# Kernel optimization log

Measured on AMD Instinct MI355X. Metric: run time of the kernel, lower is better.

The kernel has to match this reference:

```python
import jax, jax.numpy as jnp
import numpy as np

B, T, E, H = 2, 2048, 1024, 16  # batch, seq(block_size), n_embed, n_head


def setup_inputs() -> dict:
    key = jax.random.key(0)
    kx, kq, kk, kv, kf = jax.random.split(key, 5)
    s = 0.02
    return {
        "x": jax.random.normal(kx, (B, T, E), jnp.float32),
        "Wq": jax.random.normal(kq, (E, E), jnp.float32) * s,
        "Wk": jax.random.normal(kk, (E, E), jnp.float32) * s,
        "Wv": jax.random.normal(kv, (E, E), jnp.float32) * s,
        "Wf": jax.random.normal(kf, (E, E), jnp.float32) * s,
        "bf": jnp.zeros((E,), jnp.float32),
    }


def reference(x, Wq, Wk, Wv, Wf, bf):
    b, t, e = x.shape
    dh = e // H
    # per-head projections (no bias), heads concatenated along feature dim
    q = (x @ Wq).reshape(b, t, H, dh)
    k = (x @ Wk).reshape(b, t, H, dh)
    v = (x @ Wv).reshape(b, t, H, dh)
    # NOTE: original scales by sqrt(full embed dim C), not sqrt(head_size)
    scores = jnp.einsum("bqhd,bkhd->bhqk", q, k) / jnp.sqrt(jnp.asarray(e, x.dtype))
    causal = jnp.tril(jnp.ones((t, t), bool))
    scores = jnp.where(causal, scores, -jnp.inf)
    wei = jax.nn.softmax(scores, axis=-1)
    attn = jnp.einsum("bhqk,bkhd->bqhd", wei, v).reshape(b, t, e)
    x = x + attn  # residual (no out-projection in original)
    # FeedForward: single Linear + ReLU, residual
    return x + jnp.maximum(x @ Wf + bf, 0)
```

## Files before the change

kernel.cpp:

```cpp
#include <hip/hip_runtime.h>
#include <cstdint>
#include <cstddef>

typedef unsigned short u16;
typedef short short8 __attribute__((ext_vector_type(8)));
typedef float floatx4 __attribute__((ext_vector_type(4)));

__device__ __forceinline__ float bf2f(u16 u) {
    union { unsigned int i; float f; } v; v.i = ((unsigned int)u) << 16; return v.f;
}
__device__ __forceinline__ u16 f2bf(float f) {
    union { float f; unsigned int i; } v; v.f = f;
    unsigned int u = v.i;
    return (u16)((u + 0x7fffu + ((u >> 16) & 1u)) >> 16);
}

#if __has_builtin(__builtin_amdgcn_exp2f)
#define EXP2F(x) __builtin_amdgcn_exp2f(x)
#else
#define EXP2F(x) exp2f(x)
#endif

__device__ __forceinline__ void gload_lds16(const u16* g, void* lds_wave_base) {
    __builtin_amdgcn_global_load_lds(
        (__attribute__((address_space(1))) void*)g,
        (__attribute__((address_space(3))) void*)lds_wave_base,
        16, 0, 0);
}

#define WAITVM(N) asm volatile("s_waitcnt vmcnt(" #N ")" ::: "memory")
#define BARRIER_ACQ()                      \
    do {                                   \
        __builtin_amdgcn_s_barrier();      \
        asm volatile("" ::: "memory");     \
        __builtin_amdgcn_sched_barrier(0); \
    } while (0)
#define BARRIER_REL()                      \
    do {                                   \
        asm volatile("" ::: "memory");     \
        __builtin_amdgcn_s_barrier();      \
    } while (0)

__global__ void conv_transpose_k(const float* __restrict__ w0, const float* __restrict__ w1,
                                 const float* __restrict__ w2, const float* __restrict__ w3,
                                 u16* __restrict__ o0, u16* __restrict__ o1,
                                 u16* __restrict__ o2, u16* __restrict__ o3, int n) {
    __shared__ float t[32][33];
    const float* w; u16* o;
    switch (blockIdx.z) {
        case 0: w = w0; o = o0; break;
        case 1: w = w1; o = o1; break;
        case 2: w = w2; o = o2; break;
        default: w = w3; o = o3; break;
    }
    int tx = threadIdx.x, ty = threadIdx.y;
    int x0 = blockIdx.x * 32, y0 = blockIdx.y * 32;
    t[ty][tx] = w[(size_t)(y0 + ty) * n + x0 + tx];
    __syncthreads();
    o[(size_t)(x0 + ty) * n + y0 + tx] = f2bf(t[tx][ty]);
}

__global__ void conv_k(const float* __restrict__ in, u16* __restrict__ out, int n) {
    int i = (blockIdx.x * blockDim.x + threadIdx.x) * 4;
    if (i >= n) return;
    float4 v = *(const float4*)&in[i];
    ushort4 o;
    o.x = f2bf(v.x); o.y = f2bf(v.y); o.z = f2bf(v.z); o.w = f2bf(v.w);
    *(ushort4*)&out[i] = o;
}

#define QSTG(K0, BUF)                                                          \
    {                                                                          \
        _Pragma("unroll")                                                      \
        for (int it = 0; it < 2; ++it) {                                       \
            int idx = it * 256 + tid;                                          \
            int row = idx >> 2;                                                \
            int c8 = (idx & 3) * 8;                                            \
            size_t ldsoff = (size_t)(it * 256 + wave * 64) * 16;               \
            gload_lds16(&A[(size_t)(bm + row) * K + (K0) + c8],                \
                        (char*)smem + (BUF) * 8192 + ldsoff);                  \
            gload_lds16(&Bt[(size_t)(bn + row) * K + (K0) + c8],               \
                        (char*)smem + 16384 + (BUF) * 8192 + ldsoff);          \
        }                                                                      \
    }

__global__ __launch_bounds__(256, 3) void gemm_qkv(
    const u16* __restrict__ A, const u16* __restrict__ Bt,
    u16* __restrict__ qpk, u16* __restrict__ kpk, u16* __restrict__ vpk,
    int M, int T, int K) {
    __shared__ __align__(16) u16 smem[16384];

    const int tid = threadIdx.x;
    const int lane = tid & 63, wave = tid >> 6;
    const int wm = (wave >> 1) * 64, wn = (wave & 1) * 64;
    const int bm = blockIdx.x * 128, bn = blockIdx.y * 128;
    const int l15 = lane & 15, lq = lane >> 4;

    const int sec = bn >> 10;
    u16* dst = (sec == 0) ? qpk : (sec == 1) ? kpk : vpk;
    const int bnE = bn & 1023;

    floatx4 acc[4][4];
#pragma unroll
    for (int i = 0; i < 4; ++i)
#pragma unroll
        for (int j = 0; j < 4; ++j) acc[i][j] = (floatx4)0.0f;

    const int nkt = K / 32;
    QSTG(0, 0);

    for (int kt = 0; kt < nkt; ++kt) {
        const int cur = kt & 1;
        if (kt + 1 < nkt) {
            QSTG((kt + 1) * 32, cur ^ 1);
            WAITVM(4);
        } else {
            WAITVM(0);
        }
        BARRIER_ACQ();

        const u16* la = smem + cur * 4096;
        const u16* lb = smem + 8192 + cur * 4096;
        short8 af[4], bfr[4];
#pragma unroll
        for (int i = 0; i < 4; ++i) af[i] = *(const short8*)&la[(wm + i * 16 + l15) * 32 + lq * 8];
#pragma unroll
        for (int j = 0; j < 4; ++j) bfr[j] = *(const short8*)&lb[(wn + j * 16 + l15) * 32 + lq * 8];

#pragma unroll
        for (int i = 0; i < 4; ++i)
#pragma unroll
            for (int j = 0; j < 4; ++j)
                acc[i][j] = __builtin_amdgcn_mfma_f32_16x16x32_bf16(af[i], bfr[j], acc[i][j], 0, 0, 0);

        BARRIER_REL();
    }

    if (sec < 2) {
#pragma unroll
        for (int i = 0; i < 4; ++i)
#pragma unroll
            for (int r = 0; r < 4; ++r) {
                int trow = wm + i * 16 + lq * 4 + r;
                int s7 = ((trow >> 2) & 7) << 4;
#pragma unroll
                for (int j = 0; j < 4; ++j) {
                    int col = wn + j * 16 + l15;
                    smem[trow * 128 + (col ^ s7)] = f2bf(acc[i][j][r]);
                }
            }
        __syncthreads();
        const int rg = tid >> 3, cc = tid & 7;
#pragma unroll
        for (int p = 0; p < 4; ++p)
#pragma unroll
            for (int sfx = 0; sfx < 2; ++sfx) {
                int row = p * 32 + rg;
                int ch = cc + sfx * 8;
                short8 v = *(const short8*)&smem[row * 128 + ((ch * 8) ^ (((row >> 2) & 7) << 4))];
                int colE = bnE + ch * 8;
                int h = colE >> 6, d = colE & 63;
                int rowg = bm + row;
                int b = rowg >> 11, t = rowg & 2047;
                *(short8*)&dst[(((size_t)(b * 16 + h) * T) + t) * 64 + d] = v;
            }
    } else {
#pragma unroll
        for (int j = 0; j < 4; ++j) {
            int clo = wn + j * 16 + l15;
            int s7 = ((clo >> 2) & 7) << 4;
#pragma unroll
            for (int i = 0; i < 4; ++i)
#pragma unroll
                for (int r = 0; r < 4; ++r) {
                    int trow = wm + i * 16 + lq * 4 + r;
                    smem[clo * 128 + (trow ^ s7)] = f2bf(acc[i][j][r]);
                }
        }
        __syncthreads();
        const int rg = tid >> 3, cc = tid & 7;
        const int b = bm >> 11;
#pragma unroll
        for (int p = 0; p < 4; ++p)
#pragma unroll
            for (int sfx = 0; sfx < 2; ++sfx) {
                int clo = p * 32 + rg;
                int ch = cc + sfx * 8;
                short8 v = *(const short8*)&smem[clo * 128 + ((ch * 8) ^ (((clo >> 2) & 7) << 4))];
                int colE = bnE + clo;
                int h = colE >> 6, d = colE & 63;
                int t = (bm + ch * 8) & 2047;
                int kblk = t >> 6, tloc = t & 63;
                *(short8*)&dst[(((size_t)(b * 16 + h) * 32 + kblk) * 64 + d) * 64 + tloc] = v;
            }
    }
}

#define FSTG(K0, BUF)                                                          \
    {                                                                          \
        {                                                                      \
            int row = tid >> 2;                                                \
            int c8 = (tid & 3) * 8;                                            \
            size_t ldsoff = (size_t)(wave * 64) * 16;                          \
            gload_lds16(&A[(size_t)(bm + row) * K + (K0) + c8],                \
                        (char*)smemF + (BUF) * 4096 + ldsoff);                 \
        }                                                                      \
        _Pragma("unroll")                                                      \
        for (int it = 0; it < 2; ++it) {                                       \
            int idx = it * 256 + tid;                                          \
            int row = idx >> 2;                                                \
            int c8 = (idx & 3) * 8;                                            \
            size_t ldsoff = (size_t)(it * 256 + wave * 64) * 16;               \
            gload_lds16(&Bt[(size_t)(bn + row) * K + (K0) + c8],               \
                        (char*)smemF + 8192 + (BUF) * 8192 + ldsoff);          \
        }                                                                      \
    }

__global__ __launch_bounds__(256) void gemm64_bt(
    const u16* __restrict__ A, const u16* __restrict__ Bt, float* __restrict__ Cf,
    const float* __restrict__ bias, const u16* __restrict__ resid,
    int M, int N, int K) {
    __shared__ __align__(16) u16 smemF[12288];

    const int tid = threadIdx.x;
    const int lane = tid & 63, wave = tid >> 6;
    const int wm = (wave >> 1) * 32, wn = (wave & 1) * 64;
    const int bm = blockIdx.x * 64, bn = blockIdx.y * 128;
    const int l15 = lane & 15, lq = lane >> 4;

    floatx4 acc[2][4];
#pragma unroll
    for (int i = 0; i < 2; ++i)
#pragma unroll
        for (int j = 0; j < 4; ++j) acc[i][j] = (floatx4)0.0f;

    const int nkt = K / 32;
    FSTG(0, 0);

    for (int kt = 0; kt < nkt; ++kt) {
        const int cur = kt & 1;
        if (kt + 1 < nkt) {
            FSTG((kt + 1) * 32, cur ^ 1);
            WAITVM(3);
        } else {
            WAITVM(0);
        }
        BARRIER_ACQ();

        const u16* la = smemF + cur * 2048;
        const u16* lb = smemF + 4096 + cur * 2048 * 2;
        short8 af[2], bfr[4];
#pragma unroll
        for (int i = 0; i < 2; ++i) af[i] = *(const short8*)&la[(wm + i * 16 + l15) * 32 + lq * 8];
#pragma unroll
        for (int j = 0; j < 4; ++j) bfr[j] = *(const short8*)&lb[(wn + j * 16 + l15) * 32 + lq * 8];

#pragma unroll
        for (int i = 0; i < 2; ++i)
#pragma unroll
            for (int j = 0; j < 4; ++j)
                acc[i][j] = __builtin_amdgcn_mfma_f32_16x16x32_bf16(af[i], bfr[j], acc[i][j], 0, 0, 0);

        BARRIER_REL();
    }

#pragma unroll
    for (int i = 0; i < 2; ++i)
#pragma unroll
        for (int j = 0; j < 4; ++j)
#pragma unroll
            for (int r = 0; r < 4; ++r) {
                int row = bm + wm + i * 16 + lq * 4 + r;
                int col = bn + wn + j * 16 + l15;
                float v = acc[i][j][r];
                v = fmaxf(v + bias[col], 0.0f) + bf2f(resid[(size_t)row * N + col]);
                Cf[(size_t)row * N + col] = v;
            }
}

#define STAGE(KT, BUF)                                                            \
    {                                                                             \
        const u16* kc_ = kb + (size_t)((KT) * 64 + r0) * 64 + swz0;               \
        gload_lds16(kc_, (char*)kbuf + (BUF) * 8192 + wave * 1024);               \
        gload_lds16(kc_ + 32 * 64, (char*)kbuf + (BUF) * 8192 + 4096 + wave * 1024); \
        const u16* vc_ = vp + (size_t)(KT) * 4096 + r0 * 64 + swz0;               \
        gload_lds16(vc_, (char*)vbuf + (BUF) * 8192 + wave * 1024);               \
        gload_lds16(vc_ + 32 * 64, (char*)vbuf + (BUF) * 8192 + 4096 + wave * 1024); \
    }

__global__ __launch_bounds__(256) void attn11_k(
    const u16* __restrict__ qpk, const u16* __restrict__ kpk,
    const u16* __restrict__ vpack, const float* __restrict__ xf,
    u16* __restrict__ y, int T, int E) {
    __shared__ u16 kbuf[2][64 * 64];
    __shared__ u16 vbuf[2][64 * 64];

    const int tid = threadIdx.x;
    const int lane = tid & 63, wave = tid >> 6;
    const int l15 = lane & 15, lq = lane >> 4;
    const int bh = blockIdx.x;
    const int b = bh >> 4, h = bh & 15;
    const int qb = 31 - (int)blockIdx.y;

    const u16* qp = qpk + (size_t)bh * T * 64;
    const u16* kb = kpk + (size_t)bh * T * 64;
    const u16* vp = vpack + (size_t)bh * T * 64;

    const float c2 = 0.04508422f;
    const int r0 = tid >> 3;
    const int slot = tid & 7;
    const int fr0 = (r0 & 3) | (((r0 >> 3) & 1) << 2);
    const int swz0 = ((slot - fr0) & 7) * 8;

    const int rbase = ((l15 >> 2) * 8) + (l15 & 3);
    const int sA = lq + (l15 & 7);
    const int sB = lq + ((l15 & 3) | (((l15 >> 3) & 1) << 2));

    const int qt = qb * 64 + wave * 16;
    const int qg = qt + l15;
    const int nkb = qb + 1;

    short8 aq[2];
#pragma unroll
    for (int c = 0; c < 2; ++c)
        aq[c] = *(const short8*)&qp[(size_t)qg * 64 + c * 32 + lq * 8];

    floatx4 o[4];
#pragma unroll
    for (int n = 0; n < 4; ++n) o[n] = (floatx4)0.0f;
    float lsum = 0.0f;

    STAGE(0, 0);

#pragma unroll 1
    for (int kt = 0; kt < nkb; ++kt) {
        const int kc0 = kt * 64;
        const int cur = kt & 1;
        const int curoff = cur * 8192;

        if (kt + 1 < nkb) {
            STAGE(kt + 1, cur ^ 1);
            WAITVM(4);
        } else {
            WAITVM(0);
        }
        BARRIER_ACQ();

        floatx4 st[4];
        __builtin_amdgcn_s_setprio(1);
#pragma unroll
        for (int t2 = 0; t2 < 4; ++t2) {
            const int row = rbase + (t2 & 1) * 4 + (t2 >> 1) * 32;
            floatx4 sa = (floatx4)0.0f;
#pragma unroll
            for (int c = 0; c < 2; ++c) {
                int off = row * 128 + ((c * 4 + sA) & 7) * 16;
                short8 bk = *(const short8*)((const char*)kbuf + curoff + off);
                sa = __builtin_amdgcn_mfma_f32_16x16x32_bf16(bk, aq[c], sa, 0, 0, 0);
            }
            st[t2] = sa;
        }
        __builtin_amdgcn_s_setprio(0);

        const bool partial = (kt == qb);
        unsigned int pw[8];
#pragma unroll
        for (int t2 = 0; t2 < 4; ++t2) {
            float e0, e1, e2, e3;
            const int kg0 = kc0 + lq * 8 + (t2 & 1) * 4 + ((t2 >> 1) * 32);
            if (partial) {
                e0 = (kg0 + 0 <= qg) ? EXP2F(st[t2][0] * c2) : 0.0f;
                e1 = (kg0 + 1 <= qg) ? EXP2F(st[t2][1] * c2) : 0.0f;
                e2 = (kg0 + 2 <= qg) ? EXP2F(st[t2][2] * c2) : 0.0f;
                e3 = (kg0 + 3 <= qg) ? EXP2F(st[t2][3] * c2) : 0.0f;
            } else {
                e0 = EXP2F(st[t2][0] * c2);
                e1 = EXP2F(st[t2][1] * c2);
                e2 = EXP2F(st[t2][2] * c2);
                e3 = EXP2F(st[t2][3] * c2);
            }
            lsum += (e0 + e1) + (e2 + e3);
            unsigned int w0, w1;
            asm("v_cvt_pk_bf16_f32 %0, %1, %2" : "=v"(w0) : "v"(e0), "v"(e1));
            asm("v_cvt_pk_bf16_f32 %0, %1, %2" : "=v"(w1) : "v"(e2), "v"(e3));
            pw[t2 * 2 + 0] = w0;
            pw[t2 * 2 + 1] = w1;
        }

        __builtin_amdgcn_s_setprio(1);
#pragma unroll
        for (int kc = 0; kc < 2; ++kc) {
            union { unsigned int u[4]; short8 s; } ap;
            ap.u[0] = pw[kc * 4 + 0];
            ap.u[1] = pw[kc * 4 + 1];
            ap.u[2] = pw[kc * 4 + 2];
            ap.u[3] = pw[kc * 4 + 3];
#pragma unroll
            for (int n = 0; n < 4; ++n) {
                int off = (n * 16 + l15) * 128 + ((kc * 4 + sB) & 7) * 16;
                short8 bv = *(const short8*)((const char*)vbuf + curoff + off);
                o[n] = __builtin_amdgcn_mfma_f32_16x16x32_bf16(ap.s, bv, o[n], 0, 0, 0);
            }
        }
        __builtin_amdgcn_s_setprio(0);

        BARRIER_REL();
    }

    lsum += __shfl_xor(lsum, 16, 64);
    lsum += __shfl_xor(lsum, 32, 64);

    const float* xp = xf + (size_t)b * T * E + (size_t)h * 64;
    u16* yp = y + (size_t)b * T * E + (size_t)h * 64;
    float rl[4];
#pragma unroll
    for (int r = 0; r < 4; ++r) rl[r] = 1.0f / __shfl(lsum, lq * 4 + r, 64);
#pragma unroll
    for (int n = 0; n < 4; ++n)
#pragma unroll
        for (int r = 0; r < 4; ++r) {
            int rowg = qt + lq * 4 + r;
            int col = n * 16 + l15;
            float val = o[n][r] * rl[r];
            float res = __builtin_nontemporal_load(xp + (size_t)rowg * E + col);
            yp[(size_t)rowg * E + col] = f2bf(res + val);
        }
}

extern "C" void kernel_launch(void* const* d_in, const int* in_sizes, int n_in,
                              void* d_out, int out_size, void* d_ws, size_t ws_size,
                              hipStream_t stream) {
    const int B = 2, T = 2048, E = 1024;
    const int M = B * T;

    const float* x  = (const float*)d_in[0];
    const float* Wq = (const float*)d_in[1];
    const float* Wk = (const float*)d_in[2];
    const float* Wv = (const float*)d_in[3];
    const float* Wf = (const float*)d_in[4];
    const float* bf = (const float*)d_in[5];
    float* out = (float*)d_out;

    u16* ws = (u16*)d_ws;
    const size_t WN = (size_t)E * E;
    const size_t XN = (size_t)M * E;
    u16* Wqkv  = ws;
    u16* WfT   = ws + 3 * WN;
    u16* xb    = ws + 4 * WN;
    u16* qpk   = ws + 4 * WN + XN;
    u16* kpk   = ws + 4 * WN + 2 * XN;
    u16* vpk   = ws + 4 * WN + 3 * XN;
    u16* yb    = ws + 4 * WN + 4 * XN;

    conv_transpose_k<<<dim3(E / 32, E / 32, 4), dim3(32, 32), 0, stream>>>(
        Wq, Wk, Wv, Wf, Wqkv, Wqkv + WN, Wqkv + 2 * WN, WfT, E);
    conv_k<<<(int)(XN / 1024), 256, 0, stream>>>(x, xb, (int)XN);

    gemm_qkv<<<dim3(M / 128, 3 * E / 128), 256, 0, stream>>>(
        xb, Wqkv, qpk, kpk, vpk, M, T, E);

    attn11_k<<<dim3(B * 16, T / 64), 256, 0, stream>>>(qpk, kpk, vpk, x, yb, T, E);

    gemm64_bt<<<dim3(M / 64, E / 128), 256, 0, stream>>>(yb, WfT, out, bf, yb, M, E, E);
}
```

Before: 179.7 us.

## Read K/V directly from global memory in attention and fold softmax scale into Wq

The attention kernel drops its double-buffered LDS staging of K and V tiles, along with the barriers, and has each wave load its MFMA operands straight from global memory, relying on the caches for reuse across waves. The softmax scale constant is folded into the bf16 conversion of Wq, which removes a multiply before each exp2. This cuts LDS traffic and block-level synchronization, but each of the four waves now fetches the same K/V data from global memory or cache with no prefetch overlap, so load latency is exposed. Rounding Wq to bf16 after scaling also shifts precision slightly.

```diff
diff --git a/kernel.cpp b/kernel.cpp
--- a/kernel.cpp
+++ b/kernel.cpp
@@ -53,11 +53,12 @@
         case 2: w = w2; o = o2; break;
         default: w = w3; o = o3; break;
     }
+    const float sc = (blockIdx.z == 0) ? 0.04508422f : 1.0f;
     int tx = threadIdx.x, ty = threadIdx.y;
     int x0 = blockIdx.x * 32, y0 = blockIdx.y * 32;
     t[ty][tx] = w[(size_t)(y0 + ty) * n + x0 + tx];
     __syncthreads();
-    o[(size_t)(x0 + ty) * n + y0 + tx] = f2bf(t[tx][ty]);
+    o[(size_t)(x0 + ty) * n + y0 + tx] = f2bf(t[tx][ty] * sc);
 }
 
 __global__ void conv_k(const float* __restrict__ in, u16* __restrict__ out, int n) {
@@ -278,23 +279,10 @@
             }
 }
 
-#define STAGE(KT, BUF)                                                            \
-    {                                                                             \
-        const u16* kc_ = kb + (size_t)((KT) * 64 + r0) * 64 + swz0;               \
-        gload_lds16(kc_, (char*)kbuf + (BUF) * 8192 + wave * 1024);               \
-        gload_lds16(kc_ + 32 * 64, (char*)kbuf + (BUF) * 8192 + 4096 + wave * 1024); \
-        const u16* vc_ = vp + (size_t)(KT) * 4096 + r0 * 64 + swz0;               \
-        gload_lds16(vc_, (char*)vbuf + (BUF) * 8192 + wave * 1024);               \
-        gload_lds16(vc_ + 32 * 64, (char*)vbuf + (BUF) * 8192 + 4096 + wave * 1024); \
-    }
-
-__global__ __launch_bounds__(256) void attn11_k(
+__global__ __launch_bounds__(256) void attn12_k(
     const u16* __restrict__ qpk, const u16* __restrict__ kpk,
     const u16* __restrict__ vpack, const float* __restrict__ xf,
     u16* __restrict__ y, int T, int E) {
-    __shared__ u16 kbuf[2][64 * 64];
-    __shared__ u16 vbuf[2][64 * 64];
-
     const int tid = threadIdx.x;
     const int lane = tid & 63, wave = tid >> 6;
     const int l15 = lane & 15, lq = lane >> 4;
@@ -306,15 +294,7 @@
     const u16* kb = kpk + (size_t)bh * T * 64;
     const u16* vp = vpack + (size_t)bh * T * 64;
 
-    const float c2 = 0.04508422f;
-    const int r0 = tid >> 3;
-    const int slot = tid & 7;
-    const int fr0 = (r0 & 3) | (((r0 >> 3) & 1) << 2);
-    const int swz0 = ((slot - fr0) & 7) * 8;
-
     const int rbase = ((l15 >> 2) * 8) + (l15 & 3);
-    const int sA = lq + (l15 & 7);
-    const int sB = lq + ((l15 & 3) | (((l15 >> 3) & 1) << 2));
 
     const int qt = qb * 64 + wave * 16;
     const int qg = qt + l15;
@@ -330,32 +310,19 @@
     for (int n = 0; n < 4; ++n) o[n] = (floatx4)0.0f;
     float lsum = 0.0f;
 
-    STAGE(0, 0);
-
 #pragma unroll 1
     for (int kt = 0; kt < nkb; ++kt) {
         const int kc0 = kt * 64;
-        const int cur = kt & 1;
-        const int curoff = cur * 8192;
-
-        if (kt + 1 < nkb) {
-            STAGE(kt + 1, cur ^ 1);
-            WAITVM(4);
-        } else {
-            WAITVM(0);
-        }
-        BARRIER_ACQ();
 
         floatx4 st[4];
         __builtin_amdgcn_s_setprio(1);
 #pragma unroll
         for (int t2 = 0; t2 < 4; ++t2) {
-            const int row = rbase + (t2 & 1) * 4 + (t2 >> 1) * 32;
+            const int krow = kc0 + rbase + (t2 & 1) * 4 + (t2 >> 1) * 32;
             floatx4 sa = (floatx4)0.0f;
 #pragma unroll
             for (int c = 0; c < 2; ++c) {
-                int off = row * 128 + ((c * 4 + sA) & 7) * 16;
-                short8 bk = *(const short8*)((const char*)kbuf + curoff + off);
+                short8 bk = *(const short8*)&kb[(size_t)krow * 64 + c * 32 + lq * 8];
                 sa = __builtin_amdgcn_mfma_f32_16x16x32_bf16(bk, aq[c], sa, 0, 0, 0);
             }
             st[t2] = sa;
@@ -369,15 +336,15 @@
             float e0, e1, e2, e3;
             const int kg0 = kc0 + lq * 8 + (t2 & 1) * 4 + ((t2 >> 1) * 32);
             if (partial) {
-                e0 = (kg0 + 0 <= qg) ? EXP2F(st[t2][0] * c2) : 0.0f;
-                e1 = (kg0 + 1 <= qg) ? EXP2F(st[t2][1] * c2) : 0.0f;
-                e2 = (kg0 + 2 <= qg) ? EXP2F(st[t2][2] * c2) : 0.0f;
-                e3 = (kg0 + 3 <= qg) ? EXP2F(st[t2][3] * c2) : 0.0f;
+                e0 = (kg0 + 0 <= qg) ? EXP2F(st[t2][0]) : 0.0f;
+                e1 = (kg0 + 1 <= qg) ? EXP2F(st[t2][1]) : 0.0f;
+                e2 = (kg0 + 2 <= qg) ? EXP2F(st[t2][2]) : 0.0f;
+                e3 = (kg0 + 3 <= qg) ? EXP2F(st[t2][3]) : 0.0f;
             } else {
-                e0 = EXP2F(st[t2][0] * c2);
-                e1 = EXP2F(st[t2][1] * c2);
-                e2 = EXP2F(st[t2][2] * c2);
-                e3 = EXP2F(st[t2][3] * c2);
+                e0 = EXP2F(st[t2][0]);
+                e1 = EXP2F(st[t2][1]);
+                e2 = EXP2F(st[t2][2]);
+                e3 = EXP2F(st[t2][3]);
             }
             lsum += (e0 + e1) + (e2 + e3);
             unsigned int w0, w1;
@@ -397,14 +364,11 @@
             ap.u[3] = pw[kc * 4 + 3];
 #pragma unroll
             for (int n = 0; n < 4; ++n) {
-                int off = (n * 16 + l15) * 128 + ((kc * 4 + sB) & 7) * 16;
-                short8 bv = *(const short8*)((const char*)vbuf + curoff + off);
+                short8 bv = *(const short8*)&vp[(size_t)kt * 4096 + (n * 16 + l15) * 64 + kc * 32 + lq * 8];
                 o[n] = __builtin_amdgcn_mfma_f32_16x16x32_bf16(ap.s, bv, o[n], 0, 0, 0);
             }
         }
         __builtin_amdgcn_s_setprio(0);
-
-        BARRIER_REL();
     }
 
     lsum += __shfl_xor(lsum, 16, 64);
@@ -459,7 +423,7 @@
     gemm_qkv<<<dim3(M / 128, 3 * E / 128), 256, 0, stream>>>(
         xb, Wqkv, qpk, kpk, vpk, M, T, E);
 
-    attn11_k<<<dim3(B * 16, T / 64), 256, 0, stream>>>(qpk, kpk, vpk, x, yb, T, E);
+    attn12_k<<<dim3(B * 16, T / 64), 256, 0, stream>>>(qpk, kpk, vpk, x, yb, T, E);
 
     gemm64_bt<<<dim3(M / 64, E / 128), 256, 0, stream>>>(yb, WfT, out, bf, yb, M, E, E);
 }
```

New measurement: 282.8 us. +57.4%, slower.

## Double query tile per attention block and fold softmax scale into Wq

Applied to the files above, without the earlier changes.

The attention kernel now handles 128 query rows per block: each wave owns two 16-row query tiles that share every K/V tile staged in LDS, which halves K/V global traffic per query. Blocks are ordered onto a 1D grid that interleaves long and short causal ranges for load balance, and waves skip key blocks past their causal limit. The softmax scale (log2e/sqrt(E)) is folded into Wq during weight conversion, which removes a multiply per score. In exchange the kernel holds twice the accumulators in registers, and idle waves on the last tile add some imbalance.

```diff
diff --git a/kernel.cpp b/kernel.cpp
--- a/kernel.cpp
+++ b/kernel.cpp
@@ -53,11 +53,12 @@
         case 2: w = w2; o = o2; break;
         default: w = w3; o = o3; break;
     }
+    const float sc = (blockIdx.z == 0) ? 0.04508422f : 1.0f;
     int tx = threadIdx.x, ty = threadIdx.y;
     int x0 = blockIdx.x * 32, y0 = blockIdx.y * 32;
     t[ty][tx] = w[(size_t)(y0 + ty) * n + x0 + tx];
     __syncthreads();
-    o[(size_t)(x0 + ty) * n + y0 + tx] = f2bf(t[tx][ty]);
+    o[(size_t)(x0 + ty) * n + y0 + tx] = f2bf(t[tx][ty] * sc);
 }
 
 __global__ void conv_k(const float* __restrict__ in, u16* __restrict__ out, int n) {
@@ -278,7 +279,7 @@
             }
 }
 
-#define STAGE(KT, BUF)                                                            \
+#define STAGE14(KT, BUF)                                                          \
     {                                                                             \
         const u16* kc_ = kb + (size_t)((KT) * 64 + r0) * 64 + swz0;               \
         gload_lds16(kc_, (char*)kbuf + (BUF) * 8192 + wave * 1024);               \
@@ -288,7 +289,7 @@
         gload_lds16(vc_ + 32 * 64, (char*)vbuf + (BUF) * 8192 + 4096 + wave * 1024); \
     }
 
-__global__ __launch_bounds__(256) void attn11_k(
+__global__ __launch_bounds__(256) void attn14_k(
     const u16* __restrict__ qpk, const u16* __restrict__ kpk,
     const u16* __restrict__ vpack, const float* __restrict__ xf,
     u16* __restrict__ y, int T, int E) {
@@ -298,15 +299,16 @@
     const int tid = threadIdx.x;
     const int lane = tid & 63, wave = tid >> 6;
     const int l15 = lane & 15, lq = lane >> 4;
-    const int bh = blockIdx.x;
+    const int bi = blockIdx.x;
+    const int bh = bi & 31;
+    const int g = bi >> 5;
+    const int qb = (g < 8) ? (15 - g) : (g - 8);
     const int b = bh >> 4, h = bh & 15;
-    const int qb = 31 - (int)blockIdx.y;
 
     const u16* qp = qpk + (size_t)bh * T * 64;
     const u16* kb = kpk + (size_t)bh * T * 64;
     const u16* vp = vpack + (size_t)bh * T * 64;
 
-    const float c2 = 0.04508422f;
     const int r0 = tid >> 3;
     const int slot = tid & 7;
     const int fr0 = (r0 & 3) | (((r0 >> 3) & 1) << 2);
@@ -316,21 +318,25 @@
     const int sA = lq + (l15 & 7);
     const int sB = lq + ((l15 & 3) | (((l15 >> 3) & 1) << 2));
 
-    const int qt = qb * 64 + wave * 16;
-    const int qg = qt + l15;
-    const int nkb = qb + 1;
-
-    short8 aq[2];
-#pragma unroll
-    for (int c = 0; c < 2; ++c)
-        aq[c] = *(const short8*)&qp[(size_t)qg * 64 + c * 32 + lq * 8];
-
-    floatx4 o[4];
-#pragma unroll
-    for (int n = 0; n < 4; ++n) o[n] = (floatx4)0.0f;
-    float lsum = 0.0f;
-
-    STAGE(0, 0);
+    const int qt0 = qb * 128 + wave * 32;
+    const int qt1 = qt0 + 16;
+    const int qg0 = qt0 + l15, qg1 = qt1 + l15;
+    const int qmc = 2 * qb + (wave >> 1);
+    const int nkb = 2 * qb + 2;
+
+    short8 aq0[2], aq1[2];
+#pragma unroll
+    for (int c = 0; c < 2; ++c) {
+        aq0[c] = *(const short8*)&qp[(size_t)qg0 * 64 + c * 32 + lq * 8];
+        aq1[c] = *(const short8*)&qp[(size_t)qg1 * 64 + c * 32 + lq * 8];
+    }
+
+    floatx4 o0[4], o1[4];
+#pragma unroll
+    for (int n = 0; n < 4; ++n) { o0[n] = (floatx4)0.0f; o1[n] = (floatx4)0.0f; }
+    float lsum0 = 0.0f, lsum1 = 0.0f;
+
+    STAGE14(0, 0);
 
 #pragma unroll 1
     for (int kt = 0; kt < nkb; ++kt) {
@@ -339,91 +345,111 @@
         const int curoff = cur * 8192;
 
         if (kt + 1 < nkb) {
-            STAGE(kt + 1, cur ^ 1);
+            STAGE14(kt + 1, cur ^ 1);
             WAITVM(4);
         } else {
             WAITVM(0);
         }
         BARRIER_ACQ();
 
-        floatx4 st[4];
-        __builtin_amdgcn_s_setprio(1);
-#pragma unroll
-        for (int t2 = 0; t2 < 4; ++t2) {
-            const int row = rbase + (t2 & 1) * 4 + (t2 >> 1) * 32;
-            floatx4 sa = (floatx4)0.0f;
-#pragma unroll
-            for (int c = 0; c < 2; ++c) {
-                int off = row * 128 + ((c * 4 + sA) & 7) * 16;
-                short8 bk = *(const short8*)((const char*)kbuf + curoff + off);
-                sa = __builtin_amdgcn_mfma_f32_16x16x32_bf16(bk, aq[c], sa, 0, 0, 0);
-            }
-            st[t2] = sa;
-        }
-        __builtin_amdgcn_s_setprio(0);
-
-        const bool partial = (kt == qb);
-        unsigned int pw[8];
-#pragma unroll
-        for (int t2 = 0; t2 < 4; ++t2) {
-            float e0, e1, e2, e3;
-            const int kg0 = kc0 + lq * 8 + (t2 & 1) * 4 + ((t2 >> 1) * 32);
-            if (partial) {
-                e0 = (kg0 + 0 <= qg) ? EXP2F(st[t2][0] * c2) : 0.0f;
-                e1 = (kg0 + 1 <= qg) ? EXP2F(st[t2][1] * c2) : 0.0f;
-                e2 = (kg0 + 2 <= qg) ? EXP2F(st[t2][2] * c2) : 0.0f;
-                e3 = (kg0 + 3 <= qg) ? EXP2F(st[t2][3] * c2) : 0.0f;
-            } else {
-                e0 = EXP2F(st[t2][0] * c2);
-                e1 = EXP2F(st[t2][1] * c2);
-                e2 = EXP2F(st[t2][2] * c2);
-                e3 = EXP2F(st[t2][3] * c2);
-            }
-            lsum += (e0 + e1) + (e2 + e3);
-            unsigned int w0, w1;
-            asm("v_cvt_pk_bf16_f32 %0, %1, %2" : "=v"(w0) : "v"(e0), "v"(e1));
-            asm("v_cvt_pk_bf16_f32 %0, %1, %2" : "=v"(w1) : "v"(e2), "v"(e3));
-            pw[t2 * 2 + 0] = w0;
-            pw[t2 * 2 + 1] = w1;
-        }
-
-        __builtin_amdgcn_s_setprio(1);
-#pragma unroll
-        for (int kc = 0; kc < 2; ++kc) {
-            union { unsigned int u[4]; short8 s; } ap;
-            ap.u[0] = pw[kc * 4 + 0];
-            ap.u[1] = pw[kc * 4 + 1];
-            ap.u[2] = pw[kc * 4 + 2];
-            ap.u[3] = pw[kc * 4 + 3];
-#pragma unroll
-            for (int n = 0; n < 4; ++n) {
-                int off = (n * 16 + l15) * 128 + ((kc * 4 + sB) & 7) * 16;
-                short8 bv = *(const short8*)((const char*)vbuf + curoff + off);
-                o[n] = __builtin_amdgcn_mfma_f32_16x16x32_bf16(ap.s, bv, o[n], 0, 0, 0);
-            }
-        }
-        __builtin_amdgcn_s_setprio(0);
+        if (kt <= qmc) {
+            floatx4 st0[4], st1[4];
+            __builtin_amdgcn_s_setprio(1);
+#pragma unroll
+            for (int t2 = 0; t2 < 4; ++t2) {
+                const int row = rbase + (t2 & 1) * 4 + (t2 >> 1) * 32;
+                floatx4 sa0 = (floatx4)0.0f, sa1 = (floatx4)0.0f;
+#pragma unroll
+                for (int c = 0; c < 2; ++c) {
+                    int off = row * 128 + ((c * 4 + sA) & 7) * 16;
+                    short8 bk = *(const short8*)((const char*)kbuf + curoff + off);
+                    sa0 = __builtin_amdgcn_mfma_f32_16x16x32_bf16(bk, aq0[c], sa0, 0, 0, 0);
+                    sa1 = __builtin_amdgcn_mfma_f32_16x16x32_bf16(bk, aq1[c], sa1, 0, 0, 0);
+                }
+                st0[t2] = sa0; st1[t2] = sa1;
+            }
+            __builtin_amdgcn_s_setprio(0);
+
+            const bool partial = (kt == qmc);
+            unsigned int pw0[8], pw1[8];
+#pragma unroll
+            for (int t2 = 0; t2 < 4; ++t2) {
+                const int kg0 = kc0 + lq * 8 + (t2 & 1) * 4 + ((t2 >> 1) * 32);
+                float a0, a1, a2, a3, e0, e1, e2, e3;
+                if (partial) {
+                    a0 = (kg0 + 0 <= qg0) ? EXP2F(st0[t2][0]) : 0.0f;
+                    a1 = (kg0 + 1 <= qg0) ? EXP2F(st0[t2][1]) : 0.0f;
+                    a2 = (kg0 + 2 <= qg0) ? EXP2F(st0[t2][2]) : 0.0f;
+                    a3 = (kg0 + 3 <= qg0) ? EXP2F(st0[t2][3]) : 0.0f;
+                    e0 = (kg0 + 0 <= qg1) ? EXP2F(st1[t2][0]) : 0.0f;
+                    e1 = (kg0 + 1 <= qg1) ? EXP2F(st1[t2][1]) : 0.0f;
+                    e2 = (kg0 + 2 <= qg1) ? EXP2F(st1[t2][2]) : 0.0f;
+                    e3 = (kg0 + 3 <= qg1) ? EXP2F(st1[t2][3]) : 0.0f;
+                } else {
+                    a0 = EXP2F(st0[t2][0]); a1 = EXP2F(st0[t2][1]);
+                    a2 = EXP2F(st0[t2][2]); a3 = EXP2F(st0[t2][3]);
+                    e0 = EXP2F(st1[t2][0]); e1 = EXP2F(st1[t2][1]);
+                    e2 = EXP2F(st1[t2][2]); e3 = EXP2F(st1[t2][3]);
+                }
+                lsum0 += (a0 + a1) + (a2 + a3);
+                lsum1 += (e0 + e1) + (e2 + e3);
+                unsigned int w0, w1, w2, w3;
+                asm("v_cvt_pk_bf16_f32 %0, %1, %2" : "=v"(w0) : "v"(a0), "v"(a1));
+                asm("v_cvt_pk_bf16_f32 %0, %1, %2" : "=v"(w1) : "v"(a2), "v"(a3));
+                asm("v_cvt_pk_bf16_f32 %0, %1, %2" : "=v"(w2) : "v"(e0), "v"(e1));
+                asm("v_cvt_pk_bf16_f32 %0, %1, %2" : "=v"(w3) : "v"(e2), "v"(e3));
+                pw0[t2 * 2 + 0] = w0; pw0[t2 * 2 + 1] = w1;
+                pw1[t2 * 2 + 0] = w2; pw1[t2 * 2 + 1] = w3;
+            }
+
+            __builtin_amdgcn_s_setprio(1);
+#pragma unroll
+            for (int kc = 0; kc < 2; ++kc) {
+                union { unsigned int u[4]; short8 s; } ap0, ap1;
+                ap0.u[0] = pw0[kc * 4 + 0]; ap0.u[1] = pw0[kc * 4 + 1];
+                ap0.u[2] = pw0[kc * 4 + 2]; ap0.u[3] = pw0[kc * 4 + 3];
+                ap1.u[0] = pw1[kc * 4 + 0]; ap1.u[1] = pw1[kc * 4 + 1];
+                ap1.u[2] = pw1[kc * 4 + 2]; ap1.u[3] = pw1[kc * 4 + 3];
+#pragma unroll
+                for (int n = 0; n < 4; ++n) {
+                    int off = (n * 16 + l15) * 128 + ((kc * 4 + sB) & 7) * 16;
+                    short8 bv = *(const short8*)((const char*)vbuf + curoff + off);
+                    o0[n] = __builtin_amdgcn_mfma_f32_16x16x32_bf16(ap0.s, bv, o0[n], 0, 0, 0);
+                    o1[n] = __builtin_amdgcn_mfma_f32_16x16x32_bf16(ap1.s, bv, o1[n], 0, 0, 0);
+                }
+            }
+            __builtin_amdgcn_s_setprio(0);
+        }
 
         BARRIER_REL();
     }
 
-    lsum += __shfl_xor(lsum, 16, 64);
-    lsum += __shfl_xor(lsum, 32, 64);
+    lsum0 += __shfl_xor(lsum0, 16, 64);
+    lsum0 += __shfl_xor(lsum0, 32, 64);
+    lsum1 += __shfl_xor(lsum1, 16, 64);
+    lsum1 += __shfl_xor(lsum1, 32, 64);
 
     const float* xp = xf + (size_t)b * T * E + (size_t)h * 64;
     u16* yp = y + (size_t)b * T * E + (size_t)h * 64;
-    float rl[4];
-#pragma unroll
-    for (int r = 0; r < 4; ++r) rl[r] = 1.0f / __shfl(lsum, lq * 4 + r, 64);
+    float rl0[4], rl1[4];
+#pragma unroll
+    for (int r = 0; r < 4; ++r) {
+        rl0[r] = 1.0f / __shfl(lsum0, lq * 4 + r, 64);
+        rl1[r] = 1.0f / __shfl(lsum1, lq * 4 + r, 64);
+    }
 #pragma unroll
     for (int n = 0; n < 4; ++n)
 #pragma unroll
         for (int r = 0; r < 4; ++r) {
-            int rowg = qt + lq * 4 + r;
+            int row0 = qt0 + lq * 4 + r;
+            int row1 = qt1 + lq * 4 + r;
             int col = n * 16 + l15;
-            float val = o[n][r] * rl[r];
-            float res = __builtin_nontemporal_load(xp + (size_t)rowg * E + col);
-            yp[(size_t)rowg * E + col] = f2bf(res + val);
+            float v0 = o0[n][r] * rl0[r];
+            float v1 = o1[n][r] * rl1[r];
+            float x0 = __builtin_nontemporal_load(xp + (size_t)row0 * E + col);
+            float x1 = __builtin_nontemporal_load(xp + (size_t)row1 * E + col);
+            yp[(size_t)row0 * E + col] = f2bf(x0 + v0);
+            yp[(size_t)row1 * E + col] = f2bf(x1 + v1);
         }
 }
 
@@ -459,7 +485,7 @@
     gemm_qkv<<<dim3(M / 128, 3 * E / 128), 256, 0, stream>>>(
         xb, Wqkv, qpk, kpk, vpk, M, T, E);
 
-    attn11_k<<<dim3(B * 16, T / 64), 256, 0, stream>>>(qpk, kpk, vpk, x, yb, T, E);
+    attn14_k<<<dim3(512), 256, 0, stream>>>(qpk, kpk, vpk, x, yb, T, E);
 
     gemm64_bt<<<dim3(M / 64, E / 128), 256, 0, stream>>>(yb, WfT, out, bf, yb, M, E, E);
 }
```

Result: slower. 183.6 us (+2.2%).
